# Optimization experiments

Hardware: AMD Instinct MI355X
Metric: run time of the kernel (lower is better)

Reference implementation:

```python
import jax, jax.numpy as jnp
import numpy as np

B, S, D, H, FF = 4, 1024, 1024, 16, 4096
HD = D // H
SCALE = float(np.sqrt(HD))
LAMBDA_MIN = 0.5
LAMBDA_MAX = 0.5
EPS = 1e-5


def _layernorm(x, g, b):
    mu = jnp.mean(x, axis=-1, keepdims=True)
    var = jnp.mean(jnp.square(x - mu), axis=-1, keepdims=True)
    return (x - mu) * jax.lax.rsqrt(var + EPS) * g + b


def _qbnn_layer(h, W, bW, J, lam_base, g, be):
    # s_prev = tanh(h); h_tilde = h W + b; delta_j = (sum_i s_prev_i J_ij) * tanh(h_tilde)_j
    s_prev = jnp.tanh(h)
    h_tilde = h @ W + bW
    s_raw = jnp.tanh(h_tilde)
    delta = (s_prev @ J) * s_raw
    lam_n = jax.nn.sigmoid(lam_base)
    dynamic_factor = 0.5  # eval mode, call_count=0 -> 0.5+0.5*sin(0)
    lam_eff = LAMBDA_MIN + (LAMBDA_MAX - LAMBDA_MIN) * (lam_n * 0.7 + dynamic_factor * 0.3)
    h_hat = h_tilde + lam_eff * delta
    return jax.nn.gelu(_layernorm(h_hat, g, be), approximate=False)


def setup_inputs() -> dict:
    key = jax.random.key(0)
    ks = jax.random.split(key, 24)
    f32 = jnp.float32
    lin = lambda k, i, o: jax.random.normal(k, (i, o), f32) / np.sqrt(i)
    inp = {
        'x': jax.random.normal(ks[0], (B, S, D), f32),
        # attention projections (stored as [in, out]; y = x @ W + b)
        'wq': lin(ks[1], D, D), 'bq': jnp.zeros((D,), f32),
        'wk': lin(ks[2], D, D), 'bk': jnp.zeros((D,), f32),
        'wv': lin(ks[3], D, D), 'bv': jnp.zeros((D,), f32),
        'wo': lin(ks[4], D, D), 'bo': jnp.zeros((D,), f32),
        'J_attn': jax.random.normal(ks[5], (H, HD, HD), f32) * 0.02,
        'lambda_attn': jnp.asarray(0.5, f32),
        'g_attn': jnp.ones((D,), f32), 'b_attn': jnp.zeros((D,), f32),
        # ffn layer 1 (D -> FF)
        'W1': lin(ks[6], D, FF), 'b1': jnp.zeros((FF,), f32),
        'J1': jax.random.normal(ks[7], (D, FF), f32) * 0.02,
        'lam1': jnp.asarray(0.5, f32),
        'g1': jnp.ones((FF,), f32), 'be1': jnp.zeros((FF,), f32),
        # ffn layer 2 (FF -> D)
        'W2': lin(ks[8], FF, D), 'b2': jnp.zeros((D,), f32),
        'J2': jax.random.normal(ks[9], (FF, D), f32) * 0.02,
        'lam2': jnp.asarray(0.5, f32),
        'g2': jnp.ones((D,), f32), 'be2': jnp.zeros((D,), f32),
        # ffn pre-norm
        'g_ffn': jnp.ones((D,), f32), 'b_ffn': jnp.zeros((D,), f32),
    }
    return inp


def reference(x, wq, bq, wk, bk, wv, bv, wo, bo, J_attn, lambda_attn, g_attn, b_attn,
              W1, b1, J1, lam1, g1, be1, W2, b2, J2, lam2, g2, be2, g_ffn, b_ffn):
    # --- attention (pre-norm) ---
    xn = _layernorm(x, g_attn, b_attn)
    split = lambda t: t.reshape(B, S, H, HD).transpose(0, 2, 1, 3)  # bshd -> bhsd
    Q = split(xn @ wq + bq)
    K = split(xn @ wk + bk)
    V = split(xn @ wv + bv)
    scores = jnp.einsum('bhid,bhjd->bhij', Q, K) / SCALE
    tQJ = jnp.einsum('bhid,hde->bhie', jnp.tanh(Q), J_attn)
    delta = jnp.einsum('bhie,bhje->bhij', tQJ, jnp.tanh(K))
    probs = jax.nn.softmax(scores + lambda_attn * delta, axis=-1)
    attn = jnp.einsum('bhij,bhjd->bhid', probs, V)
    attn = attn.transpose(0, 2, 1, 3).reshape(B, S, D) @ wo + bo
    x = x + attn
    # --- QBNN FFN (pre-norm) ---
    h = _layernorm(x, g_ffn, b_ffn)
    h = _qbnn_layer(h, W1, b1, J1, lam1, g1, be1)
    h = _qbnn_layer(h, W2, b2, J2, lam2, g2, be2)
    return x + h
```

## Files before the change

kernel.cpp:

```cpp
#include <hip/hip_runtime.h>
#include <cmath>

typedef unsigned short u16;
typedef unsigned int   u32;
typedef short bhalf8 __attribute__((ext_vector_type(8)));
typedef float fx4    __attribute__((ext_vector_type(4)));

#define B_   4
#define S_   1024
#define D_   1024
#define H_   16
#define HD_  64
#define FF_  4096
#define NTOK (B_*S_)
#define QKVW 3072
#define LOG2E 1.44269504088896f

__device__ __forceinline__ float b2f(u16 u) {
    u32 x = ((u32)u) << 16;
    return __uint_as_float(x);
}
__device__ __forceinline__ u16 f2b(float f) {
    u32 u = __float_as_uint(f);
    u32 r = (u + 0x7fffu + ((u >> 16) & 1u)) >> 16;
    return (u16)r;
}
__device__ __forceinline__ float ftanh(float x) {
    float e = __expf(2.f * x);
    return 1.f - 2.f / (e + 1.f);
}
__device__ __forceinline__ float fexp2(float x) {
    float r;
    asm("v_exp_f32 %0, %1" : "=v"(r) : "v"(x));
    return r;
}

#define GLDS16(g, l) __builtin_amdgcn_global_load_lds( \
    (const __attribute__((address_space(1))) void*)(g), \
    (__attribute__((address_space(3))) void*)(l), 16, 0, 0)

template <int N> __device__ __forceinline__ void waitvm() {
    if constexpr (N == 8) asm volatile("s_waitcnt vmcnt(8)" ::: "memory");
    else if constexpr (N == 6) asm volatile("s_waitcnt vmcnt(6)" ::: "memory");
    else if constexpr (N == 4) asm volatile("s_waitcnt vmcnt(4)" ::: "memory");
    else if constexpr (N == 2) asm volatile("s_waitcnt vmcnt(2)" ::: "memory");
    else asm volatile("s_waitcnt vmcnt(0)" ::: "memory");
}

__device__ __forceinline__ void tile_swz(int gx, int gy, int& bx, int& by) {
    int bid = blockIdx.x;
    int nwg = gx * gy;
    if (((nwg | gy) & 7) == 0) {
        int chunk = nwg >> 3;
        int wg = (bid & 7) * chunk + (bid >> 3);
        int tps = gx << 3;
        int sup = wg / tps, rem = wg % tps;
        bx = rem >> 3;
        by = (sup << 3) + (rem & 7);
    } else {
        bx = bid % gx; by = bid / gx;
    }
}

__global__ __launch_bounds__(256) void cvt_t_k(const float* __restrict__ w0, const float* __restrict__ w1,
                                               const float* __restrict__ w2, const float* __restrict__ w3,
                                               const float* __restrict__ W1p, const float* __restrict__ J1p,
                                               const float* __restrict__ W2p, const float* __restrict__ J2p,
                                               u16* __restrict__ dst) {
    __shared__ u16 L[64][65];
    int bid = blockIdx.x, tid = threadIdx.x;
    const float* src; size_t dbase; int Kd, Nd, tk, tn;
    if (bid < 1024)      { int m = bid >> 8, t = bid & 255;
                           src = m == 0 ? w0 : m == 1 ? w1 : m == 2 ? w2 : w3;
                           dbase = (size_t)m << 20; Kd = 1024; Nd = 1024; tk = t >> 4; tn = t & 15; }
    else if (bid < 2048) { int t = bid - 1024; src = W1p; dbase = (size_t)4  << 20; Kd = 1024; Nd = 4096; tk = t >> 6; tn = t & 63; }
    else if (bid < 3072) { int t = bid - 2048; src = J1p; dbase = (size_t)8  << 20; Kd = 1024; Nd = 4096; tk = t >> 6; tn = t & 63; }
    else if (bid < 4096) { int t = bid - 3072; src = W2p; dbase = (size_t)12 << 20; Kd = 4096; Nd = 1024; tk = t >> 4; tn = t & 15; }
    else                 { int t = bid - 4096; src = J2p; dbase = (size_t)16 << 20; Kd = 4096; Nd = 1024; tk = t >> 4; tn = t & 15; }
    int k0 = tk * 64, n0 = tn * 64;
    int r = tid >> 2, c4 = (tid & 3) * 16;
    #pragma unroll
    for (int p = 0; p < 4; ++p) {
        float4 v = *(const float4*)&src[(size_t)(k0 + r) * Nd + n0 + c4 + p * 4];
        L[r][c4 + p * 4 + 0] = f2b(v.x);
        L[r][c4 + p * 4 + 1] = f2b(v.y);
        L[r][c4 + p * 4 + 2] = f2b(v.z);
        L[r][c4 + p * 4 + 3] = f2b(v.w);
    }
    __syncthreads();
    u16 o[16];
    #pragma unroll
    for (int j = 0; j < 16; ++j) o[j] = L[c4 + j][r];
    *(uint4*)&dst[dbase + (size_t)(n0 + r) * Kd + k0 + c4]     = *(uint4*)&o[0];
    *(uint4*)&dst[dbase + (size_t)(n0 + r) * Kd + k0 + c4 + 8] = *(uint4*)&o[8];
}

__global__ __launch_bounds__(256) void tanh_k(const u16* __restrict__ in, u16* __restrict__ outb) {
    size_t idx = ((size_t)blockIdx.x * 256 + threadIdx.x) * 8;
    uint4 v = *(const uint4*)&in[idx];
    const u16* p = (const u16*)&v;
    u16 o[8];
    #pragma unroll
    for (int j = 0; j < 8; ++j) o[j] = f2b(ftanh(b2f(p[j])));
    *(uint4*)&outb[idx] = *(uint4*)o;
}

template <int BM, int BN, int WM, int WN, int EPI, bool SEG>
__global__ __launch_bounds__(512, 2) void gemmP(const u16* __restrict__ A,
                                                const u16* __restrict__ Bt,
                                                const float* __restrict__ bA,
                                                const float* __restrict__ bB,
                                                const float* __restrict__ bC,
                                                const float* __restrict__ resid,
                                                void* __restrict__ Cout,
                                                int M, int N, int K) {
    constexpr int IA = BM / 128;
    constexpr int IB = BN / 128;
    constexpr int NWN = BN / WN;
    constexpr int FM = WM / 16, FN = WN / 16;
    __shared__ u16 As[4][BM * 32];
    __shared__ u16 Bs[4][BN * 32];

    const int tid = threadIdx.x;
    const int w = tid >> 6, ln = tid & 63;
    const int q = ln >> 4, mr = ln & 15;
    const int wmi = w / NWN, wni = w % NWN;
    int bx, by;
    tile_swz(N / BN, M / BM, bx, by);
    const int m0 = by * BM, n0 = bx * BN;

    const int lr = ln >> 2;
    const int sc = 8 * ((ln & 3) ^ ((ln >> 3) & 3));
    const int qx8 = 8 * (q ^ ((mr >> 1) & 3));

    const u16* aA[IA];
    const u16* aB[IB];
    #pragma unroll
    for (int i = 0; i < IA; ++i)
        aA[i] = A + (size_t)(m0 + 16 * (w + 8 * i) + lr) * K + sc;
    #pragma unroll
    for (int i = 0; i < IB; ++i)
        aB[i] = Bt + (size_t)(n0 + 16 * (w + 8 * i) + lr) * K + sc;

    fx4 acc[FM][FN];
    #pragma unroll
    for (int i = 0; i < FM; ++i)
        #pragma unroll
        for (int j = 0; j < FN; ++j) acc[i][j] = (fx4){0.f, 0.f, 0.f, 0.f};

#define GP_STAGE(slot, kk) do { \
        _Pragma("unroll") \
        for (int i = 0; i < IA; ++i) GLDS16(aA[i] + (kk), &As[slot][(16 * (w + 8 * i)) * 32]); \
        _Pragma("unroll") \
        for (int i = 0; i < IB; ++i) GLDS16(aB[i] + (kk), &Bs[slot][(16 * (w + 8 * i)) * 32]); \
    } while (0)

    const int NT = K >> 5;
    GP_STAGE(0, 0);
    GP_STAGE(1, 32);
    for (int t = 0; t < NT; ++t) {
        if (t + 2 < NT) {
            GP_STAGE((t + 2) & 3, (t + 2) << 5);
            waitvm<2 * (IA + IB)>();
        } else if (t + 1 < NT) {
            waitvm<IA + IB>();
        } else {
            waitvm<0>();
        }
        asm volatile("s_waitcnt lgkmcnt(0)" ::: "memory");
        __builtin_amdgcn_sched_barrier(0);
        __builtin_amdgcn_s_barrier();
        __builtin_amdgcn_sched_barrier(0);

        const int sl = t & 3;
        bhalf8 afr[FM], bfr[FN];
        const u16* Ap = &As[sl][0];
        const u16* Bp = &Bs[sl][0];
        #pragma unroll
        for (int fm = 0; fm < FM; ++fm)
            afr[fm] = *(const bhalf8*)&Ap[(wmi * WM + fm * 16 + mr) * 32 + qx8];
        #pragma unroll
        for (int fn = 0; fn < FN; ++fn)
            bfr[fn] = *(const bhalf8*)&Bp[(wni * WN + fn * 16 + mr) * 32 + qx8];

        __builtin_amdgcn_s_setprio(1);
        #pragma unroll
        for (int fm = 0; fm < FM; ++fm)
            #pragma unroll
            for (int fn = 0; fn < FN; ++fn)
                acc[fm][fn] = __builtin_amdgcn_mfma_f32_16x16x32_bf16(afr[fm], bfr[fn], acc[fm][fn], 0, 0, 0);
        __builtin_amdgcn_s_setprio(0);
    }
#undef GP_STAGE

    #pragma unroll
    for (int fn = 0; fn < FN; ++fn) {
        int col = n0 + wni * WN + fn * 16 + mr;
        float bs;
        if (SEG) {
            const float* bp = col < 1024 ? bA : (col < 2048 ? bB : bC);
            bs = bp[col & 1023];
        } else {
            bs = bA ? bA[col] : 0.f;
        }
        #pragma unroll
        for (int fm = 0; fm < FM; ++fm) {
            #pragma unroll
            for (int r = 0; r < 4; ++r) {
                int row    = m0 + wmi * WM + fm * 16 + q * 4 + r;
                size_t idx = (size_t)row * N + col;
                float v    = acc[fm][fn][r] + bs;
                if (EPI == 0) {
                    ((u16*)Cout)[idx] = f2b(v);
                } else if (EPI == 1) {
                    ((float*)Cout)[idx] = v + resid[idx];
                } else {
                    float ht = b2f(((u16*)Cout)[idx]);
                    ((u16*)Cout)[idx] = f2b(ht + 0.5f * v * ftanh(ht));
                }
            }
        }
    }
}

__global__ __launch_bounds__(512) void dgemmP(const u16* __restrict__ A,
                                              const u16* __restrict__ At,
                                              const u16* __restrict__ WT,
                                              const u16* __restrict__ JT,
                                              const float* __restrict__ bias,
                                              u16* __restrict__ Cout,
                                              int M, int N, int K) {
    __shared__ u16 As[4][128 * 32];
    __shared__ u16 Ts[4][128 * 32];
    __shared__ u16 Ws[4][128 * 32];
    __shared__ u16 Js[4][128 * 32];

    const int tid = threadIdx.x;
    const int w = tid >> 6, ln = tid & 63;
    const int q = ln >> 4, mr = ln & 15;
    const int wmi = w >> 2, wni = w & 3;
    int bx, by;
    tile_swz(N >> 7, M >> 7, bx, by);
    const int m0 = by * 128, n0 = bx * 128;

    const int lr = ln >> 2;
    const int sc = 8 * ((ln & 3) ^ ((ln >> 3) & 3));
    const int qx8 = 8 * (q ^ ((mr >> 1) & 3));

    const u16* aA = A  + (size_t)(m0 + 16 * w + lr) * K + sc;
    const u16* aT = At + (size_t)(m0 + 16 * w + lr) * K + sc;
    const u16* aW = WT + (size_t)(n0 + 16 * w + lr) * K + sc;
    const u16* aJ = JT + (size_t)(n0 + 16 * w + lr) * K + sc;

    fx4 aw[4][2], aj[4][2];
    #pragma unroll
    for (int i = 0; i < 4; ++i)
        #pragma unroll
        for (int j = 0; j < 2; ++j) {
            aw[i][j] = (fx4){0.f, 0.f, 0.f, 0.f};
            aj[i][j] = (fx4){0.f, 0.f, 0.f, 0.f};
        }

#define DG_STAGE(slot, kk) do { \
        GLDS16(aA + (kk), &As[slot][(16 * w) * 32]); \
        GLDS16(aT + (kk), &Ts[slot][(16 * w) * 32]); \
        GLDS16(aW + (kk), &Ws[slot][(16 * w) * 32]); \
        GLDS16(aJ + (kk), &Js[slot][(16 * w) * 32]); \
    } while (0)

    const int NT = K >> 5;
    DG_STAGE(0, 0);
    DG_STAGE(1, 32);
    for (int t = 0; t < NT; ++t) {
        if (t + 2 < NT) {
            DG_STAGE((t + 2) & 3, (t + 2) << 5);
            waitvm<8>();
        } else if (t + 1 < NT) {
            waitvm<4>();
        } else {
            waitvm<0>();
        }
        asm volatile("s_waitcnt lgkmcnt(0)" ::: "memory");
        __builtin_amdgcn_sched_barrier(0);
        __builtin_amdgcn_s_barrier();
        __builtin_amdgcn_sched_barrier(0);

        const int sl = t & 3;
        bhalf8 afr[4], tfr[4], bwf[2], bjf[2];
        #pragma unroll
        for (int fm = 0; fm < 4; ++fm) {
            afr[fm] = *(const bhalf8*)&As[sl][(wmi * 64 + fm * 16 + mr) * 32 + qx8];
            tfr[fm] = *(const bhalf8*)&Ts[sl][(wmi * 64 + fm * 16 + mr) * 32 + qx8];
        }
        #pragma unroll
        for (int fn = 0; fn < 2; ++fn) {
            bwf[fn] = *(const bhalf8*)&Ws[sl][(wni * 32 + fn * 16 + mr) * 32 + qx8];
            bjf[fn] = *(const bhalf8*)&Js[sl][(wni * 32 + fn * 16 + mr) * 32 + qx8];
        }

        __builtin_amdgcn_s_setprio(1);
        #pragma unroll
        for (int fm = 0; fm < 4; ++fm)
            #pragma unroll
            for (int fn = 0; fn < 2; ++fn) {
                aw[fm][fn] = __builtin_amdgcn_mfma_f32_16x16x32_bf16(afr[fm], bwf[fn], aw[fm][fn], 0, 0, 0);
                aj[fm][fn] = __builtin_amdgcn_mfma_f32_16x16x32_bf16(tfr[fm], bjf[fn], aj[fm][fn], 0, 0, 0);
            }
        __builtin_amdgcn_s_setprio(0);
    }
#undef DG_STAGE

    #pragma unroll
    for (int fn = 0; fn < 2; ++fn) {
        int col = n0 + wni * 32 + fn * 16 + mr;
        float bs = bias[col];
        #pragma unroll
        for (int fm = 0; fm < 4; ++fm) {
            #pragma unroll
            for (int r = 0; r < 4; ++r) {
                int row    = m0 + wmi * 64 + fm * 16 + q * 4 + r;
                size_t idx = (size_t)row * N + col;
                float ht   = aw[fm][fn][r] + bs;
                Cout[idx]  = f2b(ht + 0.5f * aj[fm][fn][r] * ftanh(ht));
            }
        }
    }
}

template <bool WT>
__global__ __launch_bounds__(256) void ln_k(const float* __restrict__ xin,
                                            const float* __restrict__ g,
                                            const float* __restrict__ bb,
                                            u16* __restrict__ out,
                                            u16* __restrict__ tout, int W) {
    __shared__ float red[8], red2[8], stats[2];
    int row = blockIdx.x, tid = threadIdx.x;
    float s = 0.f, ss = 0.f;
    for (int c = tid; c < W; c += 256) {
        float v = xin[(size_t)row * W + c];
        s += v; ss += v * v;
    }
    #pragma unroll
    for (int off = 32; off; off >>= 1) { s += __shfl_xor(s, off); ss += __shfl_xor(ss, off); }
    int wave = tid >> 6, lane = tid & 63;
    if (lane == 0) { red[wave] = s; red2[wave] = ss; }
    __syncthreads();
    if (tid == 0) {
        float S = 0.f, SS = 0.f;
        for (int w2 = 0; w2 < 4; ++w2) { S += red[w2]; SS += red2[w2]; }
        float mu = S / W;
        stats[0] = mu;
        stats[1] = rsqrtf(SS / W - mu * mu + 1e-5f);
    }
    __syncthreads();
    float mu = stats[0], rs = stats[1];
    for (int c = tid; c < W; c += 256) {
        float v = (xin[(size_t)row * W + c] - mu) * rs * g[c] + bb[c];
        out[(size_t)row * W + c] = f2b(v);
        if (WT) tout[(size_t)row * W + c] = f2b(ftanh(v));
    }
}

template <bool RES, bool OUT_F32, bool WT>
__global__ __launch_bounds__(256) void lngelu_k(const u16* __restrict__ u,
                                                const float* __restrict__ g,
                                                const float* __restrict__ be,
                                                const float* __restrict__ resid,
                                                void* __restrict__ out,
                                                u16* __restrict__ tout, int W) {
    __shared__ float ub[4096];
    __shared__ float red[8], red2[8], stats[2];
    int row = blockIdx.x, tid = threadIdx.x;
    float s = 0.f, ss = 0.f;
    for (int c = tid; c < W; c += 256) {
        float v = b2f(u[(size_t)row * W + c]);
        ub[c] = v; s += v; ss += v * v;
    }
    #pragma unroll
    for (int off = 32; off; off >>= 1) { s += __shfl_xor(s, off); ss += __shfl_xor(ss, off); }
    int wave = tid >> 6, lane = tid & 63;
    if (lane == 0) { red[wave] = s; red2[wave] = ss; }
    __syncthreads();
    if (tid == 0) {
        float S = 0.f, SS = 0.f;
        for (int w2 = 0; w2 < 4; ++w2) { S += red[w2]; SS += red2[w2]; }
        float mu = S / W;
        stats[0] = mu;
        stats[1] = rsqrtf(SS / W - mu * mu + 1e-5f);
    }
    __syncthreads();
    float mu = stats[0], rs = stats[1];
    for (int c = tid; c < W; c += 256) {
        float v = (ub[c] - mu) * rs * g[c] + be[c];
        float y = 0.5f * v * (1.f + erff(v * 0.70710678118654752f));
        if (RES) y += resid[(size_t)row * W + c];
        if (OUT_F32) ((float*)out)[(size_t)row * W + c] = y;
        else         ((u16*)out)[(size_t)row * W + c] = f2b(y);
        if (WT) tout[(size_t)row * W + c] = f2b(ftanh(y));
    }
}

__global__ __launch_bounds__(256) void aug_q_k(const u16* __restrict__ QKV,
                                               const float* __restrict__ J,
                                               const float* __restrict__ lamp,
                                               u16* __restrict__ QA) {
    __shared__ float Jl[64][68];
    __shared__ float Tq[64][65];
    int blk = blockIdx.x;
    int bh = blk >> 4, st = blk & 15;
    int b = bh >> 4, h = bh & 15;
    int s0 = st * 64;
    int tid = threadIdx.x;
    float lam = lamp[0] * LOG2E;

    for (int i = tid; i < 4096; i += 256)
        Jl[i >> 6][i & 63] = J[h * 4096 + i];
    for (int i = tid; i < 4096; i += 256) {
        int r = i >> 6, c = i & 63;
        float v  = b2f(QKV[(size_t)(b * S_ + s0 + r) * QKVW + h * 64 + c]);
        Tq[r][c] = ftanh(v);
        QA[((size_t)(bh * S_ + s0 + r)) * 128 + c] = f2b(v * (0.125f * LOG2E));
    }
    __syncthreads();

    int r = tid >> 2, c0 = (tid & 3) * 16;
    float acc[16];
    #pragma unroll
    for (int j = 0; j < 16; ++j) acc[j] = 0.f;
    for (int k = 0; k < 64; ++k) {
        float a = Tq[r][k];
        #pragma unroll
        for (int j4 = 0; j4 < 4; ++j4) {
            float4 jv = *(const float4*)&Jl[k][c0 + j4 * 4];
            acc[j4 * 4 + 0] += a * jv.x;
            acc[j4 * 4 + 1] += a * jv.y;
            acc[j4 * 4 + 2] += a * jv.z;
            acc[j4 * 4 + 3] += a * jv.w;
        }
    }
    size_t orow = ((size_t)(bh * S_ + s0 + r)) * 128 + 64 + c0;
    #pragma unroll
    for (int j = 0; j < 16; ++j) QA[orow + j] = f2b(lam * acc[j]);
}

__global__ __launch_bounds__(256) void aug_k_k(const u16* __restrict__ QKV,
                                               u16* __restrict__ KA) {
    int idx = blockIdx.x * 256 + threadIdx.x;
    int d = idx & (D_ - 1);
    int bs = idx >> 10;
    int h = d >> 6, hd = d & 63;
    int b = bs >> 10, si = bs & (S_ - 1);
    u16 v      = QKV[(size_t)bs * QKVW + 1024 + d];
    size_t row = (size_t)((b * H_ + h) * S_ + si);
    KA[row * 128 + hd]      = v;
    KA[row * 128 + 64 + hd] = f2b(ftanh(b2f(v)));
}

__global__ __launch_bounds__(256) void vt_k(const u16* __restrict__ QKV,
                                            u16* __restrict__ VT) {
    __shared__ u16 L[64][72];
    int blk = blockIdx.x;
    int bh = blk >> 4, st = blk & 15;
    int b = bh >> 4, h = bh & 15;
    int s0 = st * 64;
    int tid = threadIdx.x;
    #pragma unroll
    for (int p = 0; p < 2; ++p) {
        int i = p * 2048 + tid * 8;
        int r = i >> 6, c = i & 63;
        uint4 v = *(const uint4*)&QKV[((size_t)(b * S_ + s0 + r)) * QKVW + 2048 + h * 64 + c];
        *(uint4*)&L[r][c] = v;
    }
    __syncthreads();
    #pragma unroll
    for (int p = 0; p < 2; ++p) {
        int i = p * 2048 + tid * 8;
        int d = i >> 6, s = i & 63;
        u16 o[8];
        #pragma unroll
        for (int j = 0; j < 8; ++j) o[j] = L[s + j][d];
        *(uint4*)&VT[((size_t)(bh * 64 + d)) * S_ + s0 + s] = *(uint4*)o;
    }
}

#define QS_STRIDE 136
#define PS_STRIDE 72
__global__ __launch_bounds__(256) void attn_k(const u16* __restrict__ QA,
                                              const u16* __restrict__ KA,
                                              const u16* __restrict__ VT,
                                              u16* __restrict__ out) {
    __shared__ u16 Qs[64 * QS_STRIDE];
    __shared__ u16 Ks[2][64 * 128];
    __shared__ u16 Vs[2][64 * 64];
    __shared__ u16 Ps[64 * PS_STRIDE];

    const int tid  = threadIdx.x;
    const int w    = tid >> 6, lane = tid & 63;
    const int q    = lane >> 4, mr = lane & 15;
    const int bh   = blockIdx.x >> 4;
    const int qt   = blockIdx.x & 15;

    #pragma unroll
    for (int p = 0; p < 4; ++p) {
        int idx = p * 2048 + tid * 8;
        int row = idx >> 7, col = idx & 127;
        uint4 v4 = *(const uint4*)&QA[((size_t)(bh * S_ + qt * 64 + row)) * 128 + col];
        *(uint4*)&Qs[row * QS_STRIDE + col] = v4;
    }

#define STAGEKV(pp, kt) do { \
        _Pragma("unroll") \
        for (int i = 0; i < 4; ++i) { \
            int R = w * 16 + i * 4 + (lane >> 4); \
            GLDS16(KA + ((size_t)(bh * S_ + (kt) * 64 + R)) * 128 + 8 * ((lane & 15) ^ (R & 7)), \
                   &Ks[pp][(w * 16 + i * 4) * 128]); \
        } \
        _Pragma("unroll") \
        for (int i = 0; i < 2; ++i) { \
            int Rv = w * 16 + i * 8 + (lane >> 3); \
            GLDS16(VT + ((size_t)(bh * 64 + Rv)) * S_ + (kt) * 64 + 8 * ((lane & 7) ^ (Rv & 7)), \
                   &Vs[pp][(w * 16 + i * 8) * 64]); \
        } \
    } while (0)

    STAGEKV(0, 0);
    __syncthreads();

    bhalf8 afr[4];
    #pragma unroll
    for (int ks = 0; ks < 4; ++ks)
        afr[ks] = *(const bhalf8*)&Qs[(w * 16 + mr) * QS_STRIDE + ks * 32 + q * 8];

    fx4 zero = {0.f, 0.f, 0.f, 0.f};
    fx4 O[4] = {zero, zero, zero, zero};
    float m[4]  = {-3e38f, -3e38f, -3e38f, -3e38f};
    float l[4]  = {0.f, 0.f, 0.f, 0.f};

    int p = 0;
    for (int kt = 0; kt < 16; ++kt) {
        if (kt + 1 < 16) {
            STAGEKV(p ^ 1, kt + 1);
            waitvm<6>();
        } else {
            waitvm<0>();
        }
        __builtin_amdgcn_sched_barrier(0);
        __builtin_amdgcn_s_barrier();
        __builtin_amdgcn_sched_barrier(0);

        fx4 St[4] = {zero, zero, zero, zero};
        __builtin_amdgcn_s_setprio(1);
        #pragma unroll
        for (int nt = 0; nt < 4; ++nt) {
            #pragma unroll
            for (int ks = 0; ks < 4; ++ks) {
                bhalf8 bf = *(const bhalf8*)&Ks[p][(nt * 16 + mr) * 128 + 8 * (((ks * 4 + q) ^ (mr & 7)))];
                St[nt] = __builtin_amdgcn_mfma_f32_16x16x32_bf16(afr[ks], bf, St[nt], 0, 0, 0);
            }
        }
        __builtin_amdgcn_s_setprio(0);

        float mx[4];
        float gmx = -3e38f;
        #pragma unroll
        for (int r = 0; r < 4; ++r) {
            float v = fmaxf(fmaxf(St[0][r], St[1][r]), fmaxf(St[2][r], St[3][r]));
            #pragma unroll
            for (int off = 8; off; off >>= 1) v = fmaxf(v, __shfl_xor(v, off));
            mx[r] = v;
            gmx = fmaxf(gmx, v - m[r]);
        }
        if (!__all(gmx <= 8.f)) {
            #pragma unroll
            for (int r = 0; r < 4; ++r) {
                float nm = fmaxf(m[r], mx[r]);
                float alpha = fexp2(m[r] - nm);
                m[r] = nm;
                l[r] *= alpha;
                #pragma unroll
                for (int nt = 0; nt < 4; ++nt) O[nt][r] *= alpha;
            }
        }
        #pragma unroll
        for (int r = 0; r < 4; ++r) {
            float ps = 0.f;
            #pragma unroll
            for (int nt = 0; nt < 4; ++nt) {
                float pv = fexp2(St[nt][r] - m[r]);
                St[nt][r] = pv;
                ps += pv;
            }
            #pragma unroll
            for (int off = 8; off; off >>= 1) ps += __shfl_xor(ps, off);
            l[r] += ps;
        }
        #pragma unroll
        for (int nt = 0; nt < 4; ++nt)
            #pragma unroll
            for (int r = 0; r < 4; ++r)
                Ps[(w * 16 + q * 4 + r) * PS_STRIDE + nt * 16 + mr] = f2b(St[nt][r]);

        __builtin_amdgcn_s_setprio(1);
        #pragma unroll
        for (int ks = 0; ks < 2; ++ks) {
            bhalf8 pa = *(const bhalf8*)&Ps[(w * 16 + mr) * PS_STRIDE + ks * 32 + q * 8];
            #pragma unroll
            for (int nt = 0; nt < 4; ++nt) {
                bhalf8 bf = *(const bhalf8*)&Vs[p][(nt * 16 + mr) * 64 + 8 * (((ks * 4 + q) ^ (mr & 7)))];
                O[nt] = __builtin_amdgcn_mfma_f32_16x16x32_bf16(pa, bf, O[nt], 0, 0, 0);
            }
        }
        __builtin_amdgcn_s_setprio(0);
        asm volatile("s_waitcnt lgkmcnt(0)" ::: "memory");
        __builtin_amdgcn_sched_barrier(0);
        __builtin_amdgcn_s_barrier();
        p ^= 1;
    }
#undef STAGEKV

    const int b = bh >> 4, h = bh & 15;
    #pragma unroll
    for (int nt = 0; nt < 4; ++nt) {
        int d = nt * 16 + mr;
        #pragma unroll
        for (int r = 0; r < 4; ++r) {
            int row = qt * 64 + w * 16 + q * 4 + r;
            out[((size_t)(b * S_ + row)) * D_ + h * 64 + d] = f2b(O[nt][r] / l[r]);
        }
    }
}

extern "C" void kernel_launch(void* const* d_in, const int* in_sizes, int n_in,
                              void* d_out, int out_size, void* d_ws, size_t ws_size,
                              hipStream_t stream) {
    const float* x      = (const float*)d_in[0];
    const float* wq     = (const float*)d_in[1];
    const float* bq     = (const float*)d_in[2];
    const float* wk     = (const float*)d_in[3];
    const float* bk     = (const float*)d_in[4];
    const float* wv     = (const float*)d_in[5];
    const float* bv     = (const float*)d_in[6];
    const float* wo     = (const float*)d_in[7];
    const float* bo     = (const float*)d_in[8];
    const float* Jattn  = (const float*)d_in[9];
    const float* lamA   = (const float*)d_in[10];
    const float* g_attn = (const float*)d_in[11];
    const float* b_attn = (const float*)d_in[12];
    const float* W1     = (const float*)d_in[13];
    const float* b1     = (const float*)d_in[14];
    const float* J1     = (const float*)d_in[15];
    const float* g1     = (const float*)d_in[17];
    const float* be1    = (const float*)d_in[18];
    const float* W2     = (const float*)d_in[19];
    const float* b2     = (const float*)d_in[20];
    const float* J2     = (const float*)d_in[21];
    const float* g2     = (const float*)d_in[23];
    const float* be2    = (const float*)d_in[24];
    const float* g_ffn  = (const float*)d_in[25];
    const float* b_ffn  = (const float*)d_in[26];
    float* out = (float*)d_out;
    (void)in_sizes; (void)n_in; (void)out_size;

    char* wsp = (char*)d_ws;
    const size_t MB = 1u << 20;
    u16* WB = (u16*)(wsp);
    const u16* qkvT = WB;
    const u16* woT  = WB + ((size_t)3 << 20);
    const u16* W1T  = WB + ((size_t)4 << 20);
    const u16* J1T  = WB + ((size_t)8 << 20);
    const u16* W2T  = WB + ((size_t)12 << 20);
    const u16* J2T  = WB + ((size_t)16 << 20);
    u16*   XN   = (u16*)(wsp + 40 * MB);
    u16*   AT   = (u16*)(wsp + 40 * MB);
    u16*   Ht1  = (u16*)(wsp + 40 * MB);
    u16*   U2   = (u16*)(wsp + 40 * MB);
    u16*   QKVb = (u16*)(wsp + 48 * MB);
    u16*   Hb   = (u16*)(wsp + 48 * MB);
    float* X2   = (float*)(wsp + 56 * MB);
    u16*   QA   = (u16*)(wsp + 72 * MB);
    u16*   KA   = (u16*)(wsp + 88 * MB);
    u16*   U1   = (u16*)(wsp + 72 * MB);
    u16*   VT   = (u16*)(wsp + 104 * MB);
    u16*   Ht2  = (u16*)(wsp + 104 * MB);
    const bool dual2 = ws_size >= 136 * MB;

    dim3 blk(256), blk5(512);
    cvt_t_k<<<5120, blk, 0, stream>>>(wq, wk, wv, wo, W1, J1, W2, J2, WB);
    ln_k<false><<<NTOK, blk, 0, stream>>>(x, g_attn, b_attn, XN, nullptr, D_);
    gemmP<128, 128, 64, 32, 0, true><<<(QKVW / 128) * (NTOK / 128), blk5, 0, stream>>>(
        XN, qkvT, bq, bk, bv, nullptr, QKVb, NTOK, QKVW, D_);
    aug_q_k<<<B_ * H_ * (S_ / 64), blk, 0, stream>>>(QKVb, Jattn, lamA, QA);
    aug_k_k<<<(NTOK * D_) / 256, blk, 0, stream>>>(QKVb, KA);
    vt_k<<<B_ * H_ * (S_ / 64), blk, 0, stream>>>(QKVb, VT);
    attn_k<<<B_ * H_ * (S_ / 64), blk, 0, stream>>>(QA, KA, VT, AT);
    gemmP<128, 128, 64, 32, 1, false><<<(D_ / 128) * (NTOK / 128), blk5, 0, stream>>>(
        AT, woT, bo, nullptr, nullptr, x, X2, NTOK, D_, D_);
    ln_k<true><<<NTOK, blk, 0, stream>>>(X2, g_ffn, b_ffn, Hb, Ht1, D_);
    dgemmP<<<(FF_ / 128) * (NTOK / 128), blk5, 0, stream>>>(
        Hb, Ht1, W1T, J1T, b1, U1, NTOK, FF_, D_);
    if (dual2) {
        lngelu_k<false, false, true><<<NTOK, blk, 0, stream>>>(U1, g1, be1, nullptr, U1, Ht2, FF_);
        dgemmP<<<(D_ / 128) * (NTOK / 128), blk5, 0, stream>>>(
            U1, Ht2, W2T, J2T, b2, U2, NTOK, D_, FF_);
    } else {
        lngelu_k<false, false, false><<<NTOK, blk, 0, stream>>>(U1, g1, be1, nullptr, U1, nullptr, FF_);
        gemmP<128, 128, 64, 32, 0, false><<<(D_ / 128) * (NTOK / 128), blk5, 0, stream>>>(
            U1, W2T, b2, nullptr, nullptr, nullptr, U2, NTOK, D_, FF_);
        tanh_k<<<(NTOK * FF_) / 2048, blk, 0, stream>>>(U1, U1);
        gemmP<128, 128, 64, 32, 2, false><<<(D_ / 128) * (NTOK / 128), blk5, 0, stream>>>(
            U1, J2T, nullptr, nullptr, nullptr, nullptr, U2, NTOK, D_, FF_);
    }
    lngelu_k<true, true, false><<<NTOK, blk, 0, stream>>>(U2, g2, be2, X2, out, nullptr, D_);
}
```

Baseline: 613.0 us.

## Add 256x128 dual-GEMM kernel for FFN1 and vectorize LN-GELU loads/stores

Adds dgemmP2, a dual W/J GEMM using 256x128 output tiles with triple-buffered LDS staging and 4x4 MFMA fragments per wave. It replaces the 128x128 dgemmP for the first FFN layer, aiming for more operand reuse per LDS load and fewer blocks. The LN-GELU kernel also switches to 8-wide vectorized global loads and stores. The larger tile uses much more LDS and registers (128 accumulators per thread), which may lower occupancy.

Result: slower. 650.0 us (+6.0%).

```diff
diff --git a/kernel.cpp b/kernel.cpp
--- a/kernel.cpp
+++ b/kernel.cpp
@@ -327,6 +327,112 @@
     }
 }
 
+__global__ __launch_bounds__(512) void dgemmP2(const u16* __restrict__ A,
+                                               const u16* __restrict__ At,
+                                               const u16* __restrict__ WT,
+                                               const u16* __restrict__ JT,
+                                               const float* __restrict__ bias,
+                                               u16* __restrict__ Cout,
+                                               int M, int N, int K) {
+    __shared__ u16 As[3][256 * 32];
+    __shared__ u16 Ts[3][256 * 32];
+    __shared__ u16 Ws[3][128 * 32];
+    __shared__ u16 Js[3][128 * 32];
+
+    const int tid = threadIdx.x;
+    const int w = tid >> 6, ln = tid & 63;
+    const int q = ln >> 4, mr = ln & 15;
+    const int wmi = w >> 1, wni = w & 1;
+    int bx, by;
+    tile_swz(N >> 7, M >> 8, bx, by);
+    const int m0 = by * 256, n0 = bx * 128;
+
+    const int lr = ln >> 2;
+    const int sc = 8 * ((ln & 3) ^ ((ln >> 3) & 3));
+    const int qx8 = 8 * (q ^ ((mr >> 1) & 3));
+
+    const u16* aA0 = A  + (size_t)(m0 + 16 * w + lr) * K + sc;
+    const u16* aA1 = A  + (size_t)(m0 + 128 + 16 * w + lr) * K + sc;
+    const u16* aT0 = At + (size_t)(m0 + 16 * w + lr) * K + sc;
+    const u16* aT1 = At + (size_t)(m0 + 128 + 16 * w + lr) * K + sc;
+    const u16* aW  = WT + (size_t)(n0 + 16 * w + lr) * K + sc;
+    const u16* aJ  = JT + (size_t)(n0 + 16 * w + lr) * K + sc;
+
+    fx4 aw[4][4], aj[4][4];
+    #pragma unroll
+    for (int i = 0; i < 4; ++i)
+        #pragma unroll
+        for (int j = 0; j < 4; ++j) {
+            aw[i][j] = (fx4){0.f, 0.f, 0.f, 0.f};
+            aj[i][j] = (fx4){0.f, 0.f, 0.f, 0.f};
+        }
+
+#define DG2_STAGE(slot, kk) do { \
+        GLDS16(aA0 + (kk), &As[slot][(16 * w) * 32]); \
+        GLDS16(aA1 + (kk), &As[slot][(16 * (w + 8)) * 32]); \
+        GLDS16(aT0 + (kk), &Ts[slot][(16 * w) * 32]); \
+        GLDS16(aT1 + (kk), &Ts[slot][(16 * (w + 8)) * 32]); \
+        GLDS16(aW  + (kk), &Ws[slot][(16 * w) * 32]); \
+        GLDS16(aJ  + (kk), &Js[slot][(16 * w) * 32]); \
+    } while (0)
+
+    const int NT = K >> 5;
+    DG2_STAGE(0, 0);
+    DG2_STAGE(1, 32);
+    int sl = 0, st = 2;
+    for (int t = 0; t < NT; ++t) {
+        asm volatile("s_waitcnt lgkmcnt(0)" ::: "memory");
+        if (t + 1 < NT) waitvm<6>();
+        else            waitvm<0>();
+        __builtin_amdgcn_sched_barrier(0);
+        __builtin_amdgcn_s_barrier();
+        __builtin_amdgcn_sched_barrier(0);
+        if (t + 2 < NT) DG2_STAGE(st, (t + 2) << 5);
+
+        bhalf8 afr[4], tfr[4], bwf[4], bjf[4];
+        #pragma unroll
+        for (int fm = 0; fm < 4; ++fm) {
+            afr[fm] = *(const bhalf8*)&As[sl][(wmi * 64 + fm * 16 + mr) * 32 + qx8];
+            tfr[fm] = *(const bhalf8*)&Ts[sl][(wmi * 64 + fm * 16 + mr) * 32 + qx8];
+        }
+        #pragma unroll
+        for (int fn = 0; fn < 4; ++fn) {
+            bwf[fn] = *(const bhalf8*)&Ws[sl][(wni * 64 + fn * 16 + mr) * 32 + qx8];
+            bjf[fn] = *(const bhalf8*)&Js[sl][(wni * 64 + fn * 16 + mr) * 32 + qx8];
+        }
+
+        __builtin_amdgcn_s_setprio(1);
+        #pragma unroll
+        for (int fm = 0; fm < 4; ++fm)
+            #pragma unroll
+            for (int fn = 0; fn < 4; ++fn) {
+                aw[fm][fn] = __builtin_amdgcn_mfma_f32_16x16x32_bf16(afr[fm], bwf[fn], aw[fm][fn], 0, 0, 0);
+                aj[fm][fn] = __builtin_amdgcn_mfma_f32_16x16x32_bf16(tfr[fm], bjf[fn], aj[fm][fn], 0, 0, 0);
+            }
+        __builtin_amdgcn_s_setprio(0);
+
+        sl = sl == 2 ? 0 : sl + 1;
+        st = st == 2 ? 0 : st + 1;
+    }
+#undef DG2_STAGE
+
+    #pragma unroll
+    for (int fn = 0; fn < 4; ++fn) {
+        int col = n0 + wni * 64 + fn * 16 + mr;
+        float bs = bias[col];
+        #pragma unroll
+        for (int fm = 0; fm < 4; ++fm) {
+            #pragma unroll
+            for (int r = 0; r < 4; ++r) {
+                int row    = m0 + wmi * 64 + fm * 16 + q * 4 + r;
+                size_t idx = (size_t)row * N + col;
+                float ht   = aw[fm][fn][r] + bs;
+                Cout[idx]  = f2b(ht + 0.5f * aj[fm][fn][r] * ftanh(ht));
+            }
+        }
+    }
+}
+
 template <bool WT>
 __global__ __launch_bounds__(256) void ln_k(const float* __restrict__ xin,
                                             const float* __restrict__ g,
@@ -372,9 +478,14 @@
     __shared__ float red[8], red2[8], stats[2];
     int row = blockIdx.x, tid = threadIdx.x;
     float s = 0.f, ss = 0.f;
-    for (int c = tid; c < W; c += 256) {
-        float v = b2f(u[(size_t)row * W + c]);
-        ub[c] = v; s += v; ss += v * v;
+    for (int c = tid * 8; c < W; c += 2048) {
+        uint4 v4 = *(const uint4*)&u[(size_t)row * W + c];
+        const u16* p = (const u16*)&v4;
+        #pragma unroll
+        for (int j = 0; j < 8; ++j) {
+            float v = b2f(p[j]);
+            ub[c + j] = v; s += v; ss += v * v;
+        }
     }
     #pragma unroll
     for (int off = 32; off; off >>= 1) { s += __shfl_xor(s, off); ss += __shfl_xor(ss, off); }
@@ -390,13 +501,34 @@
     }
     __syncthreads();
     float mu = stats[0], rs = stats[1];
-    for (int c = tid; c < W; c += 256) {
-        float v = (ub[c] - mu) * rs * g[c] + be[c];
-        float y = 0.5f * v * (1.f + erff(v * 0.70710678118654752f));
-        if (RES) y += resid[(size_t)row * W + c];
-        if (OUT_F32) ((float*)out)[(size_t)row * W + c] = y;
-        else         ((u16*)out)[(size_t)row * W + c] = f2b(y);
-        if (WT) tout[(size_t)row * W + c] = f2b(ftanh(y));
+    for (int c = tid * 8; c < W; c += 2048) {
+        float y[8];
+        #pragma unroll
+        for (int j = 0; j < 8; ++j) {
+            float v = (ub[c + j] - mu) * rs * g[c + j] + be[c + j];
+            y[j] = 0.5f * v * (1.f + erff(v * 0.70710678118654752f));
+        }
+        if (RES) {
+            float4 r0 = *(const float4*)&resid[(size_t)row * W + c];
+            float4 r1 = *(const float4*)&resid[(size_t)row * W + c + 4];
+            y[0] += r0.x; y[1] += r0.y; y[2] += r0.z; y[3] += r0.w;
+            y[4] += r1.x; y[5] += r1.y; y[6] += r1.z; y[7] += r1.w;
+        }
+        if (OUT_F32) {
+            *(float4*)&((float*)out)[(size_t)row * W + c]     = (float4){y[0], y[1], y[2], y[3]};
+            *(float4*)&((float*)out)[(size_t)row * W + c + 4] = (float4){y[4], y[5], y[6], y[7]};
+        } else {
+            u16 o[8];
+            #pragma unroll
+            for (int j = 0; j < 8; ++j) o[j] = f2b(y[j]);
+            *(uint4*)&((u16*)out)[(size_t)row * W + c] = *(uint4*)o;
+        }
+        if (WT) {
+            u16 t8[8];
+            #pragma unroll
+            for (int j = 0; j < 8; ++j) t8[j] = f2b(ftanh(y[j]));
+            *(uint4*)&tout[(size_t)row * W + c] = *(uint4*)t8;
+        }
     }
 }
 
@@ -696,7 +828,7 @@
     gemmP<128, 128, 64, 32, 1, false><<<(D_ / 128) * (NTOK / 128), blk5, 0, stream>>>(
         AT, woT, bo, nullptr, nullptr, x, X2, NTOK, D_, D_);
     ln_k<true><<<NTOK, blk, 0, stream>>>(X2, g_ffn, b_ffn, Hb, Ht1, D_);
-    dgemmP<<<(FF_ / 128) * (NTOK / 128), blk5, 0, stream>>>(
+    dgemmP2<<<(FF_ / 128) * (NTOK / 256), blk5, 0, stream>>>(
         Hb, Ht1, W1T, J1T, b1, U1, NTOK, FF_, D_);
     if (dual2) {
         lngelu_k<false, false, true><<<NTOK, blk, 0, stream>>>(U1, g1, be1, nullptr, U1, Ht2, FF_);
```

## Switch dual GEMM to double-buffered LDS and vectorize LayerNorm-GELU accesses

Applied to the files above, without the earlier changes.

The dual-accumulator GEMM (h·W and tanh(h)·J) drops from a 4-slot, 2-ahead LDS pipeline to a 2-slot double buffer with a trailing barrier, halving shared memory. It also adds a launch_bounds occupancy hint of 4 blocks per CU. This trades prefetch depth for more resident blocks and adds a second barrier per K step. Separately, the LayerNorm+GELU kernel now loads and stores 8 bf16 values (or float4 pairs) per thread instead of scalar elements, to cut memory instruction count.

New measurement: 659.0 us. +7.5%, slower.

```diff
diff --git a/kernel.cpp b/kernel.cpp
--- a/kernel.cpp
+++ b/kernel.cpp
@@ -223,17 +223,17 @@
     }
 }
 
-__global__ __launch_bounds__(512) void dgemmP(const u16* __restrict__ A,
-                                              const u16* __restrict__ At,
-                                              const u16* __restrict__ WT,
-                                              const u16* __restrict__ JT,
-                                              const float* __restrict__ bias,
-                                              u16* __restrict__ Cout,
-                                              int M, int N, int K) {
-    __shared__ u16 As[4][128 * 32];
-    __shared__ u16 Ts[4][128 * 32];
-    __shared__ u16 Ws[4][128 * 32];
-    __shared__ u16 Js[4][128 * 32];
+__global__ __launch_bounds__(512, 4) void dgemmD(const u16* __restrict__ A,
+                                                 const u16* __restrict__ At,
+                                                 const u16* __restrict__ WT,
+                                                 const u16* __restrict__ JT,
+                                                 const float* __restrict__ bias,
+                                                 u16* __restrict__ Cout,
+                                                 int M, int N, int K) {
+    __shared__ u16 As[2][128 * 32];
+    __shared__ u16 Ts[2][128 * 32];
+    __shared__ u16 Ws[2][128 * 32];
+    __shared__ u16 Js[2][128 * 32];
 
     const int tid = threadIdx.x;
     const int w = tid >> 6, ln = tid & 63;
@@ -261,7 +261,7 @@
             aj[i][j] = (fx4){0.f, 0.f, 0.f, 0.f};
         }
 
-#define DG_STAGE(slot, kk) do { \
+#define DD_STAGE(slot, kk) do { \
         GLDS16(aA + (kk), &As[slot][(16 * w) * 32]); \
         GLDS16(aT + (kk), &Ts[slot][(16 * w) * 32]); \
         GLDS16(aW + (kk), &Ws[slot][(16 * w) * 32]); \
@@ -269,33 +269,29 @@
     } while (0)
 
     const int NT = K >> 5;
-    DG_STAGE(0, 0);
-    DG_STAGE(1, 32);
+    DD_STAGE(0, 0);
+    int p = 0;
     for (int t = 0; t < NT; ++t) {
-        if (t + 2 < NT) {
-            DG_STAGE((t + 2) & 3, (t + 2) << 5);
-            waitvm<8>();
-        } else if (t + 1 < NT) {
+        if (t + 1 < NT) {
+            DD_STAGE(p ^ 1, (t + 1) << 5);
             waitvm<4>();
         } else {
             waitvm<0>();
         }
-        asm volatile("s_waitcnt lgkmcnt(0)" ::: "memory");
         __builtin_amdgcn_sched_barrier(0);
         __builtin_amdgcn_s_barrier();
         __builtin_amdgcn_sched_barrier(0);
 
-        const int sl = t & 3;
         bhalf8 afr[4], tfr[4], bwf[2], bjf[2];
         #pragma unroll
         for (int fm = 0; fm < 4; ++fm) {
-            afr[fm] = *(const bhalf8*)&As[sl][(wmi * 64 + fm * 16 + mr) * 32 + qx8];
-            tfr[fm] = *(const bhalf8*)&Ts[sl][(wmi * 64 + fm * 16 + mr) * 32 + qx8];
+            afr[fm] = *(const bhalf8*)&As[p][(wmi * 64 + fm * 16 + mr) * 32 + qx8];
+            tfr[fm] = *(const bhalf8*)&Ts[p][(wmi * 64 + fm * 16 + mr) * 32 + qx8];
         }
         #pragma unroll
         for (int fn = 0; fn < 2; ++fn) {
-            bwf[fn] = *(const bhalf8*)&Ws[sl][(wni * 32 + fn * 16 + mr) * 32 + qx8];
-            bjf[fn] = *(const bhalf8*)&Js[sl][(wni * 32 + fn * 16 + mr) * 32 + qx8];
+            bwf[fn] = *(const bhalf8*)&Ws[p][(wni * 32 + fn * 16 + mr) * 32 + qx8];
+            bjf[fn] = *(const bhalf8*)&Js[p][(wni * 32 + fn * 16 + mr) * 32 + qx8];
         }
 
         __builtin_amdgcn_s_setprio(1);
@@ -307,8 +303,13 @@
                 aj[fm][fn] = __builtin_amdgcn_mfma_f32_16x16x32_bf16(tfr[fm], bjf[fn], aj[fm][fn], 0, 0, 0);
             }
         __builtin_amdgcn_s_setprio(0);
-    }
-#undef DG_STAGE
+
+        asm volatile("s_waitcnt lgkmcnt(0)" ::: "memory");
+        __builtin_amdgcn_sched_barrier(0);
+        __builtin_amdgcn_s_barrier();
+        p ^= 1;
+    }
+#undef DD_STAGE
 
     #pragma unroll
     for (int fn = 0; fn < 2; ++fn) {
@@ -372,9 +373,14 @@
     __shared__ float red[8], red2[8], stats[2];
     int row = blockIdx.x, tid = threadIdx.x;
     float s = 0.f, ss = 0.f;
-    for (int c = tid; c < W; c += 256) {
-        float v = b2f(u[(size_t)row * W + c]);
-        ub[c] = v; s += v; ss += v * v;
+    for (int c = tid * 8; c < W; c += 2048) {
+        uint4 v4 = *(const uint4*)&u[(size_t)row * W + c];
+        const u16* p = (const u16*)&v4;
+        #pragma unroll
+        for (int j = 0; j < 8; ++j) {
+            float v = b2f(p[j]);
+            ub[c + j] = v; s += v; ss += v * v;
+        }
     }
     #pragma unroll
     for (int off = 32; off; off >>= 1) { s += __shfl_xor(s, off); ss += __shfl_xor(ss, off); }
@@ -390,13 +396,34 @@
     }
     __syncthreads();
     float mu = stats[0], rs = stats[1];
-    for (int c = tid; c < W; c += 256) {
-        float v = (ub[c] - mu) * rs * g[c] + be[c];
-        float y = 0.5f * v * (1.f + erff(v * 0.70710678118654752f));
-        if (RES) y += resid[(size_t)row * W + c];
-        if (OUT_F32) ((float*)out)[(size_t)row * W + c] = y;
-        else         ((u16*)out)[(size_t)row * W + c] = f2b(y);
-        if (WT) tout[(size_t)row * W + c] = f2b(ftanh(y));
+    for (int c = tid * 8; c < W; c += 2048) {
+        float y[8];
+        #pragma unroll
+        for (int j = 0; j < 8; ++j) {
+            float v = (ub[c + j] - mu) * rs * g[c + j] + be[c + j];
+            y[j] = 0.5f * v * (1.f + erff(v * 0.70710678118654752f));
+        }
+        if (RES) {
+            float4 r0 = *(const float4*)&resid[(size_t)row * W + c];
+            float4 r1 = *(const float4*)&resid[(size_t)row * W + c + 4];
+            y[0] += r0.x; y[1] += r0.y; y[2] += r0.z; y[3] += r0.w;
+            y[4] += r1.x; y[5] += r1.y; y[6] += r1.z; y[7] += r1.w;
+        }
+        if (OUT_F32) {
+            *(float4*)&((float*)out)[(size_t)row * W + c]     = (float4){y[0], y[1], y[2], y[3]};
+            *(float4*)&((float*)out)[(size_t)row * W + c + 4] = (float4){y[4], y[5], y[6], y[7]};
+        } else {
+            u16 o[8];
+            #pragma unroll
+            for (int j = 0; j < 8; ++j) o[j] = f2b(y[j]);
+            *(uint4*)&((u16*)out)[(size_t)row * W + c] = *(uint4*)o;
+        }
+        if (WT) {
+            u16 t8[8];
+            #pragma unroll
+            for (int j = 0; j < 8; ++j) t8[j] = f2b(ftanh(y[j]));
+            *(uint4*)&tout[(size_t)row * W + c] = *(uint4*)t8;
+        }
     }
 }
 
@@ -696,11 +723,11 @@
     gemmP<128, 128, 64, 32, 1, false><<<(D_ / 128) * (NTOK / 128), blk5, 0, stream>>>(
         AT, woT, bo, nullptr, nullptr, x, X2, NTOK, D_, D_);
     ln_k<true><<<NTOK, blk, 0, stream>>>(X2, g_ffn, b_ffn, Hb, Ht1, D_);
-    dgemmP<<<(FF_ / 128) * (NTOK / 128), blk5, 0, stream>>>(
+    dgemmD<<<(FF_ / 128) * (NTOK / 128), blk5, 0, stream>>>(
         Hb, Ht1, W1T, J1T, b1, U1, NTOK, FF_, D_);
     if (dual2) {
         lngelu_k<false, false, true><<<NTOK, blk, 0, stream>>>(U1, g1, be1, nullptr, U1, Ht2, FF_);
-        dgemmP<<<(D_ / 128) * (NTOK / 128), blk5, 0, stream>>>(
+        dgemmD<<<(D_ / 128) * (NTOK / 128), blk5, 0, stream>>>(
             U1, Ht2, W2T, J2T, b2, U2, NTOK, D_, FF_);
     } else {
         lngelu_k<false, false, false><<<NTOK, blk, 0, stream>>>(U1, g1, be1, nullptr, U1, nullptr, FF_);
```
